# Kernel tuning notes

Hardware: AMD Instinct MI355X
Metric: run time of the kernel (lower is better)

The kernel has to match this reference:

```python
import jax, jax.numpy as jnp
import numpy as np

B, QL, KL = 2, 256, 256
QD, KD, H = 1024, 1024, 512
EPS = 1e-5


def setup_inputs() -> dict:
    key = jax.random.key(0)
    ks = jax.random.split(key, 12)
    s = lambda d: 1.0 / np.sqrt(d)
    return {
        "Q": jax.random.normal(ks[0], (B, QL, QD), jnp.float32),
        "K": jax.random.normal(ks[1], (B, KL, KD), jnp.float32),
        "Wq": jax.random.normal(ks[2], (H, QD), jnp.float32) * s(QD),
        "Wk": jax.random.normal(ks[3], (H, KD), jnp.float32) * s(KD),
        "ln_w": jnp.ones((3 * H,), jnp.float32),
        "ln_b": jnp.zeros((3 * H,), jnp.float32),
        "Wu": jax.random.normal(ks[4], (H, 3 * H), jnp.float32) * s(3 * H),
        "bu": jnp.zeros((H,), jnp.float32),
        "Wv": jax.random.normal(ks[5], (H, 3 * H), jnp.float32) * s(3 * H),
        "bv": jnp.zeros((H,), jnp.float32),
        "Wo": jax.random.normal(ks[6], (1, H), jnp.float32) * s(H),
        "bo": jnp.zeros((1,), jnp.float32),
    }


def reference(Q, K, Wq, Wk, ln_w, ln_b, Wu, bu, Wv, bv, Wo, bo):
    # project queries and keys to hidden
    q = jnp.einsum('bqd,hd->bqh', Q, Wq)          # (B,QL,H)
    k = jnp.einsum('bkd,hd->bkh', K, Wk)          # (B,KL,H)
    qe = jnp.broadcast_to(q[:, :, None, :], (B, QL, KL, H))
    ke = jnp.broadcast_to(k[:, None, :, :], (B, QL, KL, H))
    x = jnp.concatenate([qe, ke, qe * ke], axis=-1)   # (B,QL,KL,3H)
    # LayerNorm over last dim
    mu = jnp.mean(x, axis=-1, keepdims=True)
    var = jnp.mean((x - mu) ** 2, axis=-1, keepdims=True)
    x = (x - mu) * jax.lax.rsqrt(var + EPS) * ln_w + ln_b
    U = jnp.einsum('bqkc,hc->bqkh', x, Wu) + bu
    V = jnp.einsum('bqkc,hc->bqkh', x, Wv) + bv
    Z = U * jax.nn.gelu(V, approximate=False)
    s = jnp.einsum('bqkh,oh->bqko', Z, Wo) + bo
    return s[..., 0]                               # (B,QL,KL)
```

## Files before the change

### kernel.cpp

```cpp
#include <hip/hip_runtime.h>
#include <hip/hip_bf16.h>

#define QLEN 256
#define QD 1024
#define HD 512
#define H3 1536
#define EPSF 1e-5f

typedef __attribute__((ext_vector_type(8))) short short8;
typedef __attribute__((ext_vector_type(4))) float f32x4;

__device__ inline short f2bf(float f) {
    union { float f; unsigned u; } v; v.f = f;
    unsigned r = v.u + 0x7FFF + ((v.u >> 16) & 1);
    return (short)(r >> 16);
}
__device__ inline float bf2f(short s) {
    union { float f; unsigned u; } v; v.u = ((unsigned)(unsigned short)s) << 16;
    return v.f;
}
__device__ inline unsigned pk2(float a, float b) {
    return ((unsigned)(unsigned short)f2bf(a)) | (((unsigned)(unsigned short)f2bf(b)) << 16);
}
__device__ inline float asf(unsigned u) { union { unsigned u; float f; } v; v.u = u; return v.f; }
__device__ inline unsigned cvtpk(float lo, float hi) {
    unsigned r;
    asm("v_cvt_pk_bf16_f32 %0, %1, %2" : "=v"(r) : "v"(lo), "v"(hi));
    return r;
}

__global__ __launch_bounds__(256) void prep_w2(const float* __restrict__ Wu_, const float* __restrict__ Wv_,
                                               const float* __restrict__ lnw, const float* __restrict__ lnb,
                                               const float* __restrict__ bu_, const float* __restrict__ bv_,
                                               short* __restrict__ W1u, short* __restrict__ W2u, short* __restrict__ W3u,
                                               short* __restrict__ W1v, short* __restrict__ W2v, short* __restrict__ W3v,
                                               float* __restrict__ su, float* __restrict__ tu,
                                               float* __restrict__ sv, float* __restrict__ tv) {
    int h = blockIdx.x, z = blockIdx.y, tid = threadIdx.x;
    const float* row = (z ? Wv_ : Wu_) + (size_t)h * H3;
    const float* bias = z ? bv_ : bu_;
    short* W1 = z ? W1v : W1u; short* W2 = z ? W2v : W2u; short* W3 = z ? W3v : W3u;
    float* svec = z ? sv : su; float* tvec = z ? tv : tu;
    for (int j = tid; j < HD; j += 256) {
        W1[h * HD + j] = f2bf(lnw[j] * row[j]);
        W2[h * HD + j] = f2bf(lnw[HD + j] * row[HD + j]);
        W3[h * HD + j] = f2bf(lnw[2 * HD + j] * row[2 * HD + j]);
    }
    float s = 0.f, t = 0.f;
    for (int c = tid; c < H3; c += 256) {
        float w = row[c];
        s += lnw[c] * w;
        t += lnb[c] * w;
    }
    for (int m = 1; m < 64; m <<= 1) { s += __shfl_xor(s, m, 64); t += __shfl_xor(t, m, 64); }
    __shared__ float rs[4], rt[4];
    if ((tid & 63) == 0) { rs[tid >> 6] = s; rt[tid >> 6] = t; }
    __syncthreads();
    if (tid == 0) {
        svec[h] = rs[0] + rs[1] + rs[2] + rs[3];
        tvec[h] = rt[0] + rt[1] + rt[2] + rt[3] + bias[h];
    }
}

__global__ __launch_bounds__(256) void proj2(const float* __restrict__ Q_, const float* __restrict__ K_,
                                             const float* __restrict__ Wq_, const float* __restrict__ Wk_,
                                             short* __restrict__ qbf, short* __restrict__ kbf) {
    int z = blockIdx.z;
    const float* In = z ? K_ : Q_;
    const float* W = z ? Wk_ : Wq_;
    short* OutB = z ? kbf : qbf;
    __shared__ short a_l[64][72], b_l[64][72];
    int t = threadIdx.x;
    int i0 = blockIdx.y * 64, n0 = blockIdx.x * 64;
    int lane = t & 63, wv = t >> 6, wm = wv >> 1, wn = wv & 1;
    int l15 = lane & 15, lg = lane >> 4;
    f32x4 acc[2][2] = {};
    int sr = t >> 4, sc = (t & 15) * 4;
    for (int kc = 0; kc < QD; kc += 64) {
#pragma unroll
        for (int rep = 0; rep < 4; ++rep) {
            int row = sr + rep * 16;
            float4 av = *(const float4*)&In[(size_t)(i0 + row) * QD + kc + sc];
            float4 bv = *(const float4*)&W[(size_t)(n0 + row) * QD + kc + sc];
            *(uint2*)&a_l[row][sc] = (uint2){pk2(av.x, av.y), pk2(av.z, av.w)};
            *(uint2*)&b_l[row][sc] = (uint2){pk2(bv.x, bv.y), pk2(bv.z, bv.w)};
        }
        __syncthreads();
#pragma unroll
        for (int kk = 0; kk < 2; ++kk) {
            short8 af[2], bf_[2];
#pragma unroll
            for (int mi = 0; mi < 2; ++mi)
                af[mi] = *(const short8*)&a_l[wm * 32 + mi * 16 + l15][kk * 32 + lg * 8];
#pragma unroll
            for (int nj = 0; nj < 2; ++nj)
                bf_[nj] = *(const short8*)&b_l[wn * 32 + nj * 16 + l15][kk * 32 + lg * 8];
#pragma unroll
            for (int mi = 0; mi < 2; ++mi)
#pragma unroll
                for (int nj = 0; nj < 2; ++nj)
                    acc[mi][nj] = __builtin_amdgcn_mfma_f32_16x16x32_bf16(af[mi], bf_[nj], acc[mi][nj], 0, 0, 0);
        }
        __syncthreads();
    }
#pragma unroll
    for (int mi = 0; mi < 2; ++mi)
#pragma unroll
        for (int nj = 0; nj < 2; ++nj)
#pragma unroll
            for (int r = 0; r < 4; ++r) {
                int row = i0 + wm * 32 + mi * 16 + lg * 4 + r;
                int col = n0 + wn * 32 + nj * 16 + l15;
                OutB[(size_t)row * HD + col] = f2bf(acc[mi][nj][r]);
            }
}

__global__ __launch_bounds__(256) void rowstats2(const unsigned* __restrict__ qbf, const unsigned* __restrict__ kbf,
                                                 float* __restrict__ s1q, float* __restrict__ s2q,
                                                 float* __restrict__ s1k, float* __restrict__ s2k,
                                                 float* __restrict__ out, const float* __restrict__ bo) {
    int row = blockIdx.x, z = blockIdx.y, tid = threadIdx.x;
    int gid = (z * 512 + row) * 256 + tid;
    if (gid < 2 * QLEN * QLEN) out[gid] = bo[0];
    const unsigned* Xbf = z ? kbf : qbf;
    float* s1 = z ? s1k : s1q;
    float* s2 = z ? s2k : s2q;
    unsigned u = Xbf[row * 256 + tid];
    float a = bf2f((short)(u & 0xffff)), b = bf2f((short)(u >> 16));
    float s = a + b, q = a * a + b * b;
    for (int m = 1; m < 64; m <<= 1) { s += __shfl_xor(s, m, 64); q += __shfl_xor(q, m, 64); }
    __shared__ float rs[4], rq[4];
    if ((tid & 63) == 0) { rs[tid >> 6] = s; rq[tid >> 6] = q; }
    __syncthreads();
    if (tid == 0) {
        s1[row] = rs[0] + rs[1] + rs[2] + rs[3];
        s2[row] = rq[0] + rq[1] + rq[2] + rq[3];
    }
}

__global__ __launch_bounds__(256) void lnlin4(const short* __restrict__ qbf, const short* __restrict__ kbf,
                                              const short* __restrict__ W1u, const short* __restrict__ W1v,
                                              const short* __restrict__ W2u, const short* __restrict__ W2v,
                                              float* __restrict__ Au, float* __restrict__ Av,
                                              float* __restrict__ BuT, float* __restrict__ BvT) {
    int z = blockIdx.z;
    const short* A = (z < 2) ? qbf : kbf;
    const short* W = (z == 0) ? W1u : (z == 1) ? W1v : (z == 2) ? W2u : W2v;
    float* Out = (z == 0) ? Au : (z == 1) ? Av : (z == 2) ? BuT : BvT;
    bool tr = z >= 2;
    __shared__ short a_l[64][72], b_l[64][72];
    int t = threadIdx.x;
    int i0 = blockIdx.y * 64, n0 = blockIdx.x * 64;
    int lane = t & 63, wv = t >> 6, wm = wv >> 1, wn = wv & 1;
    int l15 = lane & 15, lg = lane >> 4;
    f32x4 acc[2][2] = {};
    int sr = t >> 4, sc = (t & 15) * 4;
    for (int kc = 0; kc < HD; kc += 64) {
#pragma unroll
        for (int rep = 0; rep < 4; ++rep) {
            int row = sr + rep * 16;
            *(uint2*)&a_l[row][sc] = *(const uint2*)&A[(size_t)(i0 + row) * HD + kc + sc];
            *(uint2*)&b_l[row][sc] = *(const uint2*)&W[(size_t)(n0 + row) * HD + kc + sc];
        }
        __syncthreads();
#pragma unroll
        for (int kk = 0; kk < 2; ++kk) {
            short8 af[2], bf_[2];
#pragma unroll
            for (int mi = 0; mi < 2; ++mi)
                af[mi] = *(const short8*)&a_l[wm * 32 + mi * 16 + l15][kk * 32 + lg * 8];
#pragma unroll
            for (int nj = 0; nj < 2; ++nj)
                bf_[nj] = *(const short8*)&b_l[wn * 32 + nj * 16 + l15][kk * 32 + lg * 8];
#pragma unroll
            for (int mi = 0; mi < 2; ++mi)
#pragma unroll
                for (int nj = 0; nj < 2; ++nj)
                    acc[mi][nj] = __builtin_amdgcn_mfma_f32_16x16x32_bf16(af[mi], bf_[nj], acc[mi][nj], 0, 0, 0);
        }
        __syncthreads();
    }
#pragma unroll
    for (int mi = 0; mi < 2; ++mi)
#pragma unroll
        for (int nj = 0; nj < 2; ++nj)
#pragma unroll
            for (int r = 0; r < 4; ++r) {
                int row = i0 + wm * 32 + mi * 16 + lg * 4 + r;
                int col = n0 + wn * 32 + nj * 16 + l15;
                if (tr) Out[(size_t)col * HD + row] = acc[mi][nj][r];
                else    Out[(size_t)row * HD + col] = acc[mi][nj][r];
            }
}

__global__ __launch_bounds__(512) void main2(const short* __restrict__ qbf,
                                             const short* __restrict__ kbf,
                                             const float* __restrict__ Au,
                                             const float* __restrict__ Av,
                                             const float* __restrict__ BuT,
                                             const float* __restrict__ BvT,
                                             const short* __restrict__ W3u,
                                             const short* __restrict__ W3v,
                                             const float* __restrict__ su,
                                             const float* __restrict__ tu,
                                             const float* __restrict__ sv,
                                             const float* __restrict__ tv,
                                             const float* __restrict__ Wo,
                                             const float* __restrict__ s1q,
                                             const float* __restrict__ s2q,
                                             const float* __restrict__ s1k,
                                             const float* __restrict__ s2k,
                                             float* __restrict__ out) {
    __shared__ short q_l[16 * 512];
    __shared__ short k_l[16 * 512];
    __shared__ short B_l[2][2][128 * 64];
    __shared__ float stat_l[512];
    __shared__ float sred[8][64];

    int tid = threadIdx.x;
    int kt = blockIdx.x, qt = blockIdx.y;
    int b = blockIdx.z >> 2, hs = blockIdx.z & 3;
    int qbase = qt * 16, kbase = kt * 16, hbase = hs * 128;
    int lane = tid & 63, wv = tid >> 6;
    int l15 = lane & 15, lg = lane >> 4;
    int wm = wv & 3, wn = wv >> 2;

    f32x4 accU[4][4], accV[4][4];
#pragma unroll
    for (int mf = 0; mf < 4; ++mf) {
        int qrow = b * QLEN + qbase + wm * 4 + mf;
#pragma unroll
        for (int nf = 0; nf < 4; ++nf) {
            int h = hbase + wn * 64 + nf * 16 + l15;
            float au = Au[(size_t)qrow * HD + h];
            float av = Av[(size_t)qrow * HD + h];
            f32x4 bu4 = *(const f32x4*)&BuT[(size_t)h * 512 + b * QLEN + kbase + lg * 4];
            f32x4 bv4 = *(const f32x4*)&BvT[(size_t)h * 512 + b * QLEN + kbase + lg * 4];
#pragma unroll
            for (int r = 0; r < 4; ++r) {
                accU[mf][nf][r] = au + bu4[r];
                accV[mf][nf][r] = av + bv4[r];
            }
        }
    }

    stat_l[tid] = 0.f;
    for (int i = tid; i < 2048; i += 512) {
        int tile = i >> 10, slot = i & 1023;
        int row = slot >> 6, col16 = slot & 63;
        const short* sp = (tile ? kbf : qbf) +
            (size_t)(b * QLEN + (tile ? kbase : qbase) + row) * HD + col16 * 8;
        uint4 v = *(const uint4*)sp;
        short* dl = tile ? k_l : q_l;
        unsigned off = row * 1024 + ((col16 * 16) ^ ((row & 7) << 4));
        *(uint4*)((char*)dl + off) = v;
    }

    uint4 rb[4];
    auto loadB = [&](int kc) {
#pragma unroll
        for (int s = 0; s < 4; ++s) {
            int idx = s * 512 + tid;
            int uvx = idx >> 10, in = idx & 1023;
            int r = in >> 3, c16 = in & 7;
            const short* src = (uvx ? W3v : W3u) + (size_t)(hbase + r) * HD + kc + c16 * 8;
            rb[s] = *(const uint4*)src;
        }
    };
    auto storeB = [&](int buf) {
#pragma unroll
        for (int s = 0; s < 4; ++s) {
            int idx = s * 512 + tid;
            int uvx = idx >> 10, in = idx & 1023;
            int r = in >> 3, c16 = in & 7;
            unsigned off = r * 128 + ((c16 * 16) ^ ((r & 7) << 4));
            *(uint4*)((char*)&B_l[buf][uvx][0] + off) = rb[s];
        }
    };

    loadB(0);

    for (int c = 0; c < 8; ++c) {
        storeB(c & 1);
        if (c < 7) loadB((c + 1) * 64);
        __syncthreads();

        if (c == 0) {
            f32x4 d1 = {0.f, 0.f, 0.f, 0.f}, d2 = {0.f, 0.f, 0.f, 0.f};
#pragma unroll
            for (int s = 0; s < 2; ++s) {
                int jb = (wv * 2 + s) * 64 + lg * 16;
                uint4 qfu = *(const uint4*)((const char*)q_l + l15 * 1024 + (jb ^ ((l15 & 7) << 4)));
                uint4 kfu = *(const uint4*)((const char*)k_l + l15 * 1024 + (jb ^ ((l15 & 7) << 4)));
                d1 = __builtin_amdgcn_mfma_f32_16x16x32_bf16(
                    *(short8*)&qfu, *(short8*)&kfu, d1, 0, 0, 0);
                uint4 q2u, k2u;
                unsigned* qp = (unsigned*)&qfu; unsigned* kp = (unsigned*)&kfu;
                unsigned* q2p = (unsigned*)&q2u; unsigned* k2p = (unsigned*)&k2u;
#pragma unroll
                for (int i = 0; i < 4; ++i) {
                    float ql = asf(qp[i] << 16), qh = asf(qp[i] & 0xFFFF0000u);
                    float kl = asf(kp[i] << 16), kh = asf(kp[i] & 0xFFFF0000u);
                    q2p[i] = cvtpk(ql * ql, qh * qh);
                    k2p[i] = cvtpk(kl * kl, kh * kh);
                }
                d2 = __builtin_amdgcn_mfma_f32_16x16x32_bf16(
                    *(short8*)&q2u, *(short8*)&k2u, d2, 0, 0, 0);
            }
#pragma unroll
            for (int r = 0; r < 4; ++r) {
                int p = (lg * 4 + r) * 16 + l15;
                atomicAdd(&stat_l[p], d1[r]);
                atomicAdd(&stat_l[256 + p], d2[r]);
            }
        }

        const char* blu = (const char*)&B_l[c & 1][0][0];
        const char* blv = (const char*)&B_l[c & 1][1][0];
#pragma unroll
        for (int ksub = 0; ksub < 2; ++ksub) {
            int jb = (c * 2 + ksub) * 64 + lg * 16;
            int bb = ksub * 64 + lg * 16;
            uint4 kfu = *(const uint4*)((const char*)k_l + l15 * 1024 + (jb ^ ((l15 & 7) << 4)));
            unsigned* kp = (unsigned*)&kfu;
            float klo[4], khi[4];
#pragma unroll
            for (int i = 0; i < 4; ++i) {
                klo[i] = asf(kp[i] << 16);
                khi[i] = asf(kp[i] & 0xFFFF0000u);
            }
            short8 af[4];
#pragma unroll
            for (int mf = 0; mf < 4; ++mf) {
                int qrow = wm * 4 + mf;
                uint4 qfu = *(const uint4*)((const char*)q_l + qrow * 1024 + (jb ^ ((qrow & 7) << 4)));
                unsigned* qp = (unsigned*)&qfu;
                uint4 afu;
                unsigned* ap = (unsigned*)&afu;
#pragma unroll
                for (int i = 0; i < 4; ++i) {
                    float ql = asf(qp[i] << 16), qh = asf(qp[i] & 0xFFFF0000u);
                    ap[i] = cvtpk(ql * klo[i], qh * khi[i]);
                }
                af[mf] = *(short8*)&afu;
            }
#pragma unroll
            for (int nf = 0; nf < 4; ++nf) {
                int row = wn * 64 + nf * 16 + l15;
                unsigned off = row * 128 + (bb ^ ((row & 7) << 4));
                short8 bu_f = *(const short8*)(blu + off);
                short8 bv_f = *(const short8*)(blv + off);
#pragma unroll
                for (int mf = 0; mf < 4; ++mf) {
                    accU[mf][nf] = __builtin_amdgcn_mfma_f32_16x16x32_bf16(af[mf], bu_f, accU[mf][nf], 0, 0, 0);
                    accV[mf][nf] = __builtin_amdgcn_mfma_f32_16x16x32_bf16(af[mf], bv_f, accV[mf][nf], 0, 0, 0);
                }
            }
        }
    }

    if (tid < 256) {
        int qi = tid >> 4, ki = tid & 15;
        float mu = (s1q[b * QLEN + qbase + qi] + s1k[b * QLEN + kbase + ki] + stat_l[tid]) * (1.f / H3);
        float ex2 = (s2q[b * QLEN + qbase + qi] + s2k[b * QLEN + kbase + ki] + stat_l[256 + tid]) * (1.f / H3);
        float ri = rsqrtf(ex2 - mu * mu + EPSF);
        stat_l[tid] = ri;
        stat_l[256 + tid] = ri * mu;
    }
    __syncthreads();

    float sacc[16];
#pragma unroll
    for (int i = 0; i < 16; ++i) sacc[i] = 0.f;
#pragma unroll
    for (int nf = 0; nf < 4; ++nf) {
        int h = hbase + wn * 64 + nf * 16 + l15;
        float suh = su[h], tuh = tu[h], svh = sv[h], tvh = tv[h], woh = Wo[h];
#pragma unroll
        for (int mf = 0; mf < 4; ++mf) {
            int pbase = (wm * 4 + mf) * 16 + lg * 4;
#pragma unroll
            for (int r = 0; r < 4; ++r) {
                float ri = stat_l[pbase + r];
                float rmu = stat_l[256 + pbase + r];
                float u = fmaf(ri, accU[mf][nf][r], tuh) - rmu * suh;
                float vx = fmaf(ri, accV[mf][nf][r], tvh) - rmu * svh;
                float x2 = vx * vx;
                float tt = vx * fmaf(0.0356774081f, x2, 0.7978845608f);
                float e2 = exp2f(tt * 2.885390082f);
                float ge = vx - vx / (e2 + 1.0f);
                sacc[mf * 4 + r] = fmaf(u * ge, woh, sacc[mf * 4 + r]);
            }
        }
    }

#pragma unroll
    for (int i = 0; i < 16; ++i) {
        float v = sacc[i];
        v += __shfl_xor(v, 1, 64);
        v += __shfl_xor(v, 2, 64);
        v += __shfl_xor(v, 4, 64);
        v += __shfl_xor(v, 8, 64);
        sacc[i] = v;
    }
    if (l15 == 0) {
#pragma unroll
        for (int mf = 0; mf < 4; ++mf)
#pragma unroll
            for (int r = 0; r < 4; ++r)
                sred[wv][mf * 16 + lg * 4 + r] = sacc[mf * 4 + r];
    }
    __syncthreads();
    if (tid < 256) {
        int wm_ = tid >> 6, within = tid & 63;
        float val = sred[wm_][within] + sred[wm_ + 4][within];
        int qi = wm_ * 4 + (within >> 4), ki = within & 15;
        atomicAdd(&out[(size_t)(b * QLEN + qbase + qi) * QLEN + kbase + ki], val);
    }
}

extern "C" void kernel_launch(void* const* d_in, const int* in_sizes, int n_in,
                              void* d_out, int out_size, void* d_ws, size_t ws_size,
                              hipStream_t stream) {
    const float* Q   = (const float*)d_in[0];
    const float* Kin = (const float*)d_in[1];
    const float* Wq  = (const float*)d_in[2];
    const float* Wk  = (const float*)d_in[3];
    const float* lnw = (const float*)d_in[4];
    const float* lnb = (const float*)d_in[5];
    const float* Wu  = (const float*)d_in[6];
    const float* bu  = (const float*)d_in[7];
    const float* Wv  = (const float*)d_in[8];
    const float* bv  = (const float*)d_in[9];
    const float* Wo  = (const float*)d_in[10];
    const float* bo  = (const float*)d_in[11];
    float* out = (float*)d_out;

    char* ws = (char*)d_ws;
    size_t off = 0;
    auto alloc = [&](size_t bytes) -> void* {
        void* p = ws + off;
        off += (bytes + 255) & ~(size_t)255;
        return p;
    };
    const size_t WB = (size_t)HD * HD * 2;
    short* W1u = (short*)alloc(WB); short* W2u = (short*)alloc(WB); short* W3u = (short*)alloc(WB);
    short* W1v = (short*)alloc(WB); short* W2v = (short*)alloc(WB); short* W3v = (short*)alloc(WB);
    short* qbf = (short*)alloc(WB); short* kbf = (short*)alloc(WB);
    float* su = (float*)alloc(HD * 4); float* tu = (float*)alloc(HD * 4);
    float* sv = (float*)alloc(HD * 4); float* tv = (float*)alloc(HD * 4);
    float* s1q = (float*)alloc(512 * 4); float* s2q = (float*)alloc(512 * 4);
    float* s1k = (float*)alloc(512 * 4); float* s2k = (float*)alloc(512 * 4);
    float* Au  = (float*)alloc((size_t)512 * HD * 4);
    float* Av  = (float*)alloc((size_t)512 * HD * 4);
    float* BuT = (float*)alloc((size_t)512 * HD * 4);
    float* BvT = (float*)alloc((size_t)512 * HD * 4);

    prep_w2<<<dim3(HD, 2), 256, 0, stream>>>(Wu, Wv, lnw, lnb, bu, bv,
                                             W1u, W2u, W3u, W1v, W2v, W3v, su, tu, sv, tv);

    proj2<<<dim3(8, 8, 2), 256, 0, stream>>>(Q, Kin, Wq, Wk, qbf, kbf);

    rowstats2<<<dim3(512, 2), 256, 0, stream>>>((const unsigned*)qbf, (const unsigned*)kbf,
                                                s1q, s2q, s1k, s2k, out, bo);

    lnlin4<<<dim3(8, 8, 4), 256, 0, stream>>>(qbf, kbf, W1u, W1v, W2u, W2v, Au, Av, BuT, BvT);

    main2<<<dim3(16, 16, 8), 512, 0, stream>>>(
        qbf, kbf, Au, Av, BuT, BvT, W3u, W3v, su, tu, sv, tv, Wo,
        s1q, s2q, s1k, s2k, out);
}
```

Measured before the change: 433.2 us.

## Switch to fp16 with packed products and pre-swizzled W3 fragments read directly

Changes every intermediate from bf16 to fp16. The q*k elementwise product is now a native packed half multiply instead of unpack, float multiply and repack. W3 is pre-permuted in prep into the MFMA fragment layout, so main2 reads B fragments straight from global memory, with no LDS staging, double buffering or syncs. The Au/Av/BuT/BvT loads move into the epilogue. fp16 has less range than bf16, and squared values or products could overflow, which is a risk for accuracy.

```diff
diff --git a/kernel.cpp b/kernel.cpp
--- a/kernel.cpp
+++ b/kernel.cpp
@@ -7,44 +7,34 @@
 #define H3 1536
 #define EPSF 1e-5f
 
-typedef __attribute__((ext_vector_type(8))) short short8;
+typedef __attribute__((ext_vector_type(8))) _Float16 half8;
 typedef __attribute__((ext_vector_type(4))) float f32x4;
 
-__device__ inline short f2bf(float f) {
-    union { float f; unsigned u; } v; v.f = f;
-    unsigned r = v.u + 0x7FFF + ((v.u >> 16) & 1);
-    return (short)(r >> 16);
-}
-__device__ inline float bf2f(short s) {
-    union { float f; unsigned u; } v; v.u = ((unsigned)(unsigned short)s) << 16;
-    return v.f;
-}
-__device__ inline unsigned pk2(float a, float b) {
-    return ((unsigned)(unsigned short)f2bf(a)) | (((unsigned)(unsigned short)f2bf(b)) << 16);
-}
-__device__ inline float asf(unsigned u) { union { unsigned u; float f; } v; v.u = u; return v.f; }
-__device__ inline unsigned cvtpk(float lo, float hi) {
-    unsigned r;
-    asm("v_cvt_pk_bf16_f32 %0, %1, %2" : "=v"(r) : "v"(lo), "v"(hi));
-    return r;
+__device__ inline short f2h(float f) { _Float16 h = (_Float16)f; return __builtin_bit_cast(short, h); }
+__device__ inline float h2f(short s) { return (float)__builtin_bit_cast(_Float16, s); }
+__device__ inline unsigned pkh(float a, float b) {
+    return __builtin_bit_cast(unsigned, __builtin_amdgcn_cvt_pkrtz(a, b));
 }
 
 __global__ __launch_bounds__(256) void prep_w2(const float* __restrict__ Wu_, const float* __restrict__ Wv_,
                                                const float* __restrict__ lnw, const float* __restrict__ lnb,
                                                const float* __restrict__ bu_, const float* __restrict__ bv_,
-                                               short* __restrict__ W1u, short* __restrict__ W2u, short* __restrict__ W3u,
-                                               short* __restrict__ W1v, short* __restrict__ W2v, short* __restrict__ W3v,
+                                               short* __restrict__ W1u, short* __restrict__ W2u, short* __restrict__ W3pu,
+                                               short* __restrict__ W1v, short* __restrict__ W2v, short* __restrict__ W3pv,
                                                float* __restrict__ su, float* __restrict__ tu,
                                                float* __restrict__ sv, float* __restrict__ tv) {
     int h = blockIdx.x, z = blockIdx.y, tid = threadIdx.x;
     const float* row = (z ? Wv_ : Wu_) + (size_t)h * H3;
     const float* bias = z ? bv_ : bu_;
-    short* W1 = z ? W1v : W1u; short* W2 = z ? W2v : W2u; short* W3 = z ? W3v : W3u;
+    short* W1 = z ? W1v : W1u; short* W2 = z ? W2v : W2u; short* W3p = z ? W3pv : W3pu;
     float* svec = z ? sv : su; float* tvec = z ? tv : tu;
+    int ht = h >> 4, l15h = h & 15;
     for (int j = tid; j < HD; j += 256) {
-        W1[h * HD + j] = f2bf(lnw[j] * row[j]);
-        W2[h * HD + j] = f2bf(lnw[HD + j] * row[HD + j]);
-        W3[h * HD + j] = f2bf(lnw[2 * HD + j] * row[2 * HD + j]);
+        W1[h * HD + j] = f2h(lnw[j] * row[j]);
+        W2[h * HD + j] = f2h(lnw[HD + j] * row[HD + j]);
+        float w3 = lnw[2 * HD + j] * row[2 * HD + j];
+        int ks = j >> 5, lg2 = (j >> 3) & 3, ii = j & 7;
+        W3p[((ht * 16 + ks) * 64 + lg2 * 16 + l15h) * 8 + ii] = f2h(w3);
     }
     float s = 0.f, t = 0.f;
     for (int c = tid; c < H3; c += 256) {
@@ -64,11 +54,11 @@
 
 __global__ __launch_bounds__(256) void proj2(const float* __restrict__ Q_, const float* __restrict__ K_,
                                              const float* __restrict__ Wq_, const float* __restrict__ Wk_,
-                                             short* __restrict__ qbf, short* __restrict__ kbf) {
+                                             short* __restrict__ qh, short* __restrict__ kh) {
     int z = blockIdx.z;
     const float* In = z ? K_ : Q_;
     const float* W = z ? Wk_ : Wq_;
-    short* OutB = z ? kbf : qbf;
+    short* OutB = z ? kh : qh;
     __shared__ short a_l[64][72], b_l[64][72];
     int t = threadIdx.x;
     int i0 = blockIdx.y * 64, n0 = blockIdx.x * 64;
@@ -82,24 +72,24 @@
             int row = sr + rep * 16;
             float4 av = *(const float4*)&In[(size_t)(i0 + row) * QD + kc + sc];
             float4 bv = *(const float4*)&W[(size_t)(n0 + row) * QD + kc + sc];
-            *(uint2*)&a_l[row][sc] = (uint2){pk2(av.x, av.y), pk2(av.z, av.w)};
-            *(uint2*)&b_l[row][sc] = (uint2){pk2(bv.x, bv.y), pk2(bv.z, bv.w)};
+            *(uint2*)&a_l[row][sc] = (uint2){pkh(av.x, av.y), pkh(av.z, av.w)};
+            *(uint2*)&b_l[row][sc] = (uint2){pkh(bv.x, bv.y), pkh(bv.z, bv.w)};
         }
         __syncthreads();
 #pragma unroll
         for (int kk = 0; kk < 2; ++kk) {
-            short8 af[2], bf_[2];
+            half8 af[2], bf_[2];
 #pragma unroll
             for (int mi = 0; mi < 2; ++mi)
-                af[mi] = *(const short8*)&a_l[wm * 32 + mi * 16 + l15][kk * 32 + lg * 8];
+                af[mi] = *(const half8*)&a_l[wm * 32 + mi * 16 + l15][kk * 32 + lg * 8];
 #pragma unroll
             for (int nj = 0; nj < 2; ++nj)
-                bf_[nj] = *(const short8*)&b_l[wn * 32 + nj * 16 + l15][kk * 32 + lg * 8];
+                bf_[nj] = *(const half8*)&b_l[wn * 32 + nj * 16 + l15][kk * 32 + lg * 8];
 #pragma unroll
             for (int mi = 0; mi < 2; ++mi)
 #pragma unroll
                 for (int nj = 0; nj < 2; ++nj)
-                    acc[mi][nj] = __builtin_amdgcn_mfma_f32_16x16x32_bf16(af[mi], bf_[nj], acc[mi][nj], 0, 0, 0);
+                    acc[mi][nj] = __builtin_amdgcn_mfma_f32_16x16x32_f16(af[mi], bf_[nj], acc[mi][nj], 0, 0, 0);
         }
         __syncthreads();
     }
@@ -111,22 +101,22 @@
             for (int r = 0; r < 4; ++r) {
                 int row = i0 + wm * 32 + mi * 16 + lg * 4 + r;
                 int col = n0 + wn * 32 + nj * 16 + l15;
-                OutB[(size_t)row * HD + col] = f2bf(acc[mi][nj][r]);
+                OutB[(size_t)row * HD + col] = f2h(acc[mi][nj][r]);
             }
 }
 
-__global__ __launch_bounds__(256) void rowstats2(const unsigned* __restrict__ qbf, const unsigned* __restrict__ kbf,
+__global__ __launch_bounds__(256) void rowstats2(const unsigned* __restrict__ qh, const unsigned* __restrict__ kh,
                                                  float* __restrict__ s1q, float* __restrict__ s2q,
                                                  float* __restrict__ s1k, float* __restrict__ s2k,
                                                  float* __restrict__ out, const float* __restrict__ bo) {
     int row = blockIdx.x, z = blockIdx.y, tid = threadIdx.x;
     int gid = (z * 512 + row) * 256 + tid;
     if (gid < 2 * QLEN * QLEN) out[gid] = bo[0];
-    const unsigned* Xbf = z ? kbf : qbf;
+    const unsigned* Xh = z ? kh : qh;
     float* s1 = z ? s1k : s1q;
     float* s2 = z ? s2k : s2q;
-    unsigned u = Xbf[row * 256 + tid];
-    float a = bf2f((short)(u & 0xffff)), b = bf2f((short)(u >> 16));
+    unsigned u = Xh[row * 256 + tid];
+    float a = h2f((short)(u & 0xffff)), b = h2f((short)(u >> 16));
     float s = a + b, q = a * a + b * b;
     for (int m = 1; m < 64; m <<= 1) { s += __shfl_xor(s, m, 64); q += __shfl_xor(q, m, 64); }
     __shared__ float rs[4], rq[4];
@@ -138,13 +128,13 @@
     }
 }
 
-__global__ __launch_bounds__(256) void lnlin4(const short* __restrict__ qbf, const short* __restrict__ kbf,
+__global__ __launch_bounds__(256) void lnlin4(const short* __restrict__ qh, const short* __restrict__ kh,
                                               const short* __restrict__ W1u, const short* __restrict__ W1v,
                                               const short* __restrict__ W2u, const short* __restrict__ W2v,
                                               float* __restrict__ Au, float* __restrict__ Av,
                                               float* __restrict__ BuT, float* __restrict__ BvT) {
     int z = blockIdx.z;
-    const short* A = (z < 2) ? qbf : kbf;
+    const short* A = (z < 2) ? qh : kh;
     const short* W = (z == 0) ? W1u : (z == 1) ? W1v : (z == 2) ? W2u : W2v;
     float* Out = (z == 0) ? Au : (z == 1) ? Av : (z == 2) ? BuT : BvT;
     bool tr = z >= 2;
@@ -165,18 +155,18 @@
         __syncthreads();
 #pragma unroll
         for (int kk = 0; kk < 2; ++kk) {
-            short8 af[2], bf_[2];
+            half8 af[2], bf_[2];
 #pragma unroll
             for (int mi = 0; mi < 2; ++mi)
-                af[mi] = *(const short8*)&a_l[wm * 32 + mi * 16 + l15][kk * 32 + lg * 8];
+                af[mi] = *(const half8*)&a_l[wm * 32 + mi * 16 + l15][kk * 32 + lg * 8];
 #pragma unroll
             for (int nj = 0; nj < 2; ++nj)
-                bf_[nj] = *(const short8*)&b_l[wn * 32 + nj * 16 + l15][kk * 32 + lg * 8];
+                bf_[nj] = *(const half8*)&b_l[wn * 32 + nj * 16 + l15][kk * 32 + lg * 8];
 #pragma unroll
             for (int mi = 0; mi < 2; ++mi)
 #pragma unroll
                 for (int nj = 0; nj < 2; ++nj)
-                    acc[mi][nj] = __builtin_amdgcn_mfma_f32_16x16x32_bf16(af[mi], bf_[nj], acc[mi][nj], 0, 0, 0);
+                    acc[mi][nj] = __builtin_amdgcn_mfma_f32_16x16x32_f16(af[mi], bf_[nj], acc[mi][nj], 0, 0, 0);
         }
         __syncthreads();
     }
@@ -193,14 +183,14 @@
             }
 }
 
-__global__ __launch_bounds__(512) void main2(const short* __restrict__ qbf,
-                                             const short* __restrict__ kbf,
+__global__ __launch_bounds__(512) void main2(const short* __restrict__ qh,
+                                             const short* __restrict__ kh,
                                              const float* __restrict__ Au,
                                              const float* __restrict__ Av,
                                              const float* __restrict__ BuT,
                                              const float* __restrict__ BvT,
-                                             const short* __restrict__ W3u,
-                                             const short* __restrict__ W3v,
+                                             const short* __restrict__ W3pu,
+                                             const short* __restrict__ W3pv,
                                              const float* __restrict__ su,
                                              const float* __restrict__ tu,
                                              const float* __restrict__ sv,
@@ -213,7 +203,6 @@
                                              float* __restrict__ out) {
     __shared__ short q_l[16 * 512];
     __shared__ short k_l[16 * 512];
-    __shared__ short B_l[2][2][128 * 64];
     __shared__ float stat_l[512];
     __shared__ float sred[8][64];
 
@@ -225,140 +214,68 @@
     int l15 = lane & 15, lg = lane >> 4;
     int wm = wv & 3, wn = wv >> 2;
 
-    f32x4 accU[4][4], accV[4][4];
-#pragma unroll
-    for (int mf = 0; mf < 4; ++mf) {
-        int qrow = b * QLEN + qbase + wm * 4 + mf;
-#pragma unroll
-        for (int nf = 0; nf < 4; ++nf) {
-            int h = hbase + wn * 64 + nf * 16 + l15;
-            float au = Au[(size_t)qrow * HD + h];
-            float av = Av[(size_t)qrow * HD + h];
-            f32x4 bu4 = *(const f32x4*)&BuT[(size_t)h * 512 + b * QLEN + kbase + lg * 4];
-            f32x4 bv4 = *(const f32x4*)&BvT[(size_t)h * 512 + b * QLEN + kbase + lg * 4];
-#pragma unroll
-            for (int r = 0; r < 4; ++r) {
-                accU[mf][nf][r] = au + bu4[r];
-                accV[mf][nf][r] = av + bv4[r];
-            }
-        }
-    }
-
     stat_l[tid] = 0.f;
     for (int i = tid; i < 2048; i += 512) {
         int tile = i >> 10, slot = i & 1023;
         int row = slot >> 6, col16 = slot & 63;
-        const short* sp = (tile ? kbf : qbf) +
+        const short* sp = (tile ? kh : qh) +
             (size_t)(b * QLEN + (tile ? kbase : qbase) + row) * HD + col16 * 8;
         uint4 v = *(const uint4*)sp;
         short* dl = tile ? k_l : q_l;
         unsigned off = row * 1024 + ((col16 * 16) ^ ((row & 7) << 4));
         *(uint4*)((char*)dl + off) = v;
     }
-
-    uint4 rb[4];
-    auto loadB = [&](int kc) {
-#pragma unroll
-        for (int s = 0; s < 4; ++s) {
-            int idx = s * 512 + tid;
-            int uvx = idx >> 10, in = idx & 1023;
-            int r = in >> 3, c16 = in & 7;
-            const short* src = (uvx ? W3v : W3u) + (size_t)(hbase + r) * HD + kc + c16 * 8;
-            rb[s] = *(const uint4*)src;
-        }
-    };
-    auto storeB = [&](int buf) {
-#pragma unroll
-        for (int s = 0; s < 4; ++s) {
-            int idx = s * 512 + tid;
-            int uvx = idx >> 10, in = idx & 1023;
-            int r = in >> 3, c16 = in & 7;
-            unsigned off = r * 128 + ((c16 * 16) ^ ((r & 7) << 4));
-            *(uint4*)((char*)&B_l[buf][uvx][0] + off) = rb[s];
-        }
-    };
-
-    loadB(0);
-
-    for (int c = 0; c < 8; ++c) {
-        storeB(c & 1);
-        if (c < 7) loadB((c + 1) * 64);
-        __syncthreads();
-
-        if (c == 0) {
-            f32x4 d1 = {0.f, 0.f, 0.f, 0.f}, d2 = {0.f, 0.f, 0.f, 0.f};
-#pragma unroll
-            for (int s = 0; s < 2; ++s) {
-                int jb = (wv * 2 + s) * 64 + lg * 16;
-                uint4 qfu = *(const uint4*)((const char*)q_l + l15 * 1024 + (jb ^ ((l15 & 7) << 4)));
-                uint4 kfu = *(const uint4*)((const char*)k_l + l15 * 1024 + (jb ^ ((l15 & 7) << 4)));
-                d1 = __builtin_amdgcn_mfma_f32_16x16x32_bf16(
-                    *(short8*)&qfu, *(short8*)&kfu, d1, 0, 0, 0);
-                uint4 q2u, k2u;
-                unsigned* qp = (unsigned*)&qfu; unsigned* kp = (unsigned*)&kfu;
-                unsigned* q2p = (unsigned*)&q2u; unsigned* k2p = (unsigned*)&k2u;
-#pragma unroll
-                for (int i = 0; i < 4; ++i) {
-                    float ql = asf(qp[i] << 16), qh = asf(qp[i] & 0xFFFF0000u);
-                    float kl = asf(kp[i] << 16), kh = asf(kp[i] & 0xFFFF0000u);
-                    q2p[i] = cvtpk(ql * ql, qh * qh);
-                    k2p[i] = cvtpk(kl * kl, kh * kh);
-                }
-                d2 = __builtin_amdgcn_mfma_f32_16x16x32_bf16(
-                    *(short8*)&q2u, *(short8*)&k2u, d2, 0, 0, 0);
+    __syncthreads();
+
+    {
+        f32x4 d1 = {0.f, 0.f, 0.f, 0.f}, d2 = {0.f, 0.f, 0.f, 0.f};
+#pragma unroll
+        for (int s = 0; s < 2; ++s) {
+            int jb = (wv * 2 + s) * 64 + lg * 16;
+            uint4 qfu = *(const uint4*)((const char*)q_l + l15 * 1024 + (jb ^ ((l15 & 7) << 4)));
+            uint4 kfu = *(const uint4*)((const char*)k_l + l15 * 1024 + (jb ^ ((l15 & 7) << 4)));
+            half8 q8 = __builtin_bit_cast(half8, qfu);
+            half8 k8 = __builtin_bit_cast(half8, kfu);
+            half8 q2 = q8 * q8, k2 = k8 * k8;
+            d1 = __builtin_amdgcn_mfma_f32_16x16x32_f16(q8, k8, d1, 0, 0, 0);
+            d2 = __builtin_amdgcn_mfma_f32_16x16x32_f16(q2, k2, d2, 0, 0, 0);
+        }
+#pragma unroll
+        for (int r = 0; r < 4; ++r) {
+            int p = (lg * 4 + r) * 16 + l15;
+            atomicAdd(&stat_l[p], d1[r]);
+            atomicAdd(&stat_l[256 + p], d2[r]);
+        }
+    }
+
+    f32x4 accU[4][4] = {}, accV[4][4] = {};
+    int ht0 = hs * 8 + wn * 4;
+#pragma unroll 2
+    for (int ks = 0; ks < 16; ++ks) {
+        int jb = ks * 64 + lg * 16;
+        uint4 kfu = *(const uint4*)((const char*)k_l + l15 * 1024 + (jb ^ ((l15 & 7) << 4)));
+        half8 k8 = __builtin_bit_cast(half8, kfu);
+        half8 af[4];
+#pragma unroll
+        for (int mf = 0; mf < 4; ++mf) {
+            int qrow = wm * 4 + mf;
+            uint4 qfu = *(const uint4*)((const char*)q_l + qrow * 1024 + (jb ^ ((qrow & 7) << 4)));
+            af[mf] = __builtin_bit_cast(half8, qfu) * k8;
+        }
+#pragma unroll
+        for (int nf = 0; nf < 4; ++nf) {
+            int fo = ((ht0 + nf) * 16 + ks) * 512 + lane * 8;
+            half8 bu = *(const half8*)(W3pu + fo);
+            half8 bv = *(const half8*)(W3pv + fo);
+#pragma unroll
+            for (int mf = 0; mf < 4; ++mf) {
+                accU[mf][nf] = __builtin_amdgcn_mfma_f32_16x16x32_f16(af[mf], bu, accU[mf][nf], 0, 0, 0);
+                accV[mf][nf] = __builtin_amdgcn_mfma_f32_16x16x32_f16(af[mf], bv, accV[mf][nf], 0, 0, 0);
             }
-#pragma unroll
-            for (int r = 0; r < 4; ++r) {
-                int p = (lg * 4 + r) * 16 + l15;
-                atomicAdd(&stat_l[p], d1[r]);
-                atomicAdd(&stat_l[256 + p], d2[r]);
-            }
-        }
-
-        const char* blu = (const char*)&B_l[c & 1][0][0];
-        const char* blv = (const char*)&B_l[c & 1][1][0];
-#pragma unroll
-        for (int ksub = 0; ksub < 2; ++ksub) {
-            int jb = (c * 2 + ksub) * 64 + lg * 16;
-            int bb = ksub * 64 + lg * 16;
-            uint4 kfu = *(const uint4*)((const char*)k_l + l15 * 1024 + (jb ^ ((l15 & 7) << 4)));
-            unsigned* kp = (unsigned*)&kfu;
-            float klo[4], khi[4];
-#pragma unroll
-            for (int i = 0; i < 4; ++i) {
-                klo[i] = asf(kp[i] << 16);
-                khi[i] = asf(kp[i] & 0xFFFF0000u);
-            }
-            short8 af[4];
-#pragma unroll
-            for (int mf = 0; mf < 4; ++mf) {
-                int qrow = wm * 4 + mf;
-                uint4 qfu = *(const uint4*)((const char*)q_l + qrow * 1024 + (jb ^ ((qrow & 7) << 4)));
-                unsigned* qp = (unsigned*)&qfu;
-                uint4 afu;
-                unsigned* ap = (unsigned*)&afu;
-#pragma unroll
-                for (int i = 0; i < 4; ++i) {
-                    float ql = asf(qp[i] << 16), qh = asf(qp[i] & 0xFFFF0000u);
-                    ap[i] = cvtpk(ql * klo[i], qh * khi[i]);
-                }
-                af[mf] = *(short8*)&afu;
-            }
-#pragma unroll
-            for (int nf = 0; nf < 4; ++nf) {
-                int row = wn * 64 + nf * 16 + l15;
-                unsigned off = row * 128 + (bb ^ ((row & 7) << 4));
-                short8 bu_f = *(const short8*)(blu + off);
-                short8 bv_f = *(const short8*)(blv + off);
-#pragma unroll
-                for (int mf = 0; mf < 4; ++mf) {
-                    accU[mf][nf] = __builtin_amdgcn_mfma_f32_16x16x32_bf16(af[mf], bu_f, accU[mf][nf], 0, 0, 0);
-                    accV[mf][nf] = __builtin_amdgcn_mfma_f32_16x16x32_bf16(af[mf], bv_f, accV[mf][nf], 0, 0, 0);
-                }
-            }
-        }
-    }
-
+        }
+    }
+
+    __syncthreads();
     if (tid < 256) {
         int qi = tid >> 4, ki = tid & 15;
         float mu = (s1q[b * QLEN + qbase + qi] + s1k[b * QLEN + kbase + ki] + stat_l[tid]) * (1.f / H3);
@@ -376,15 +293,22 @@
     for (int nf = 0; nf < 4; ++nf) {
         int h = hbase + wn * 64 + nf * 16 + l15;
         float suh = su[h], tuh = tu[h], svh = sv[h], tvh = tv[h], woh = Wo[h];
+        f32x4 bu4 = *(const f32x4*)&BuT[(size_t)h * 512 + b * QLEN + kbase + lg * 4];
+        f32x4 bv4 = *(const f32x4*)&BvT[(size_t)h * 512 + b * QLEN + kbase + lg * 4];
 #pragma unroll
         for (int mf = 0; mf < 4; ++mf) {
+            int qrow = b * QLEN + qbase + wm * 4 + mf;
+            float au = Au[(size_t)qrow * HD + h];
+            float av = Av[(size_t)qrow * HD + h];
             int pbase = (wm * 4 + mf) * 16 + lg * 4;
 #pragma unroll
             for (int r = 0; r < 4; ++r) {
                 float ri = stat_l[pbase + r];
                 float rmu = stat_l[256 + pbase + r];
-                float u = fmaf(ri, accU[mf][nf][r], tuh) - rmu * suh;
-                float vx = fmaf(ri, accV[mf][nf][r], tvh) - rmu * svh;
+                float gu = au + bu4[r] + accU[mf][nf][r];
+                float gv = av + bv4[r] + accV[mf][nf][r];
+                float u = fmaf(ri, gu, tuh) - rmu * suh;
+                float vx = fmaf(ri, gv, tvh) - rmu * svh;
                 float x2 = vx * vx;
                 float tt = vx * fmaf(0.0356774081f, x2, 0.7978845608f);
                 float e2 = exp2f(tt * 2.885390082f);
@@ -444,9 +368,9 @@
         return p;
     };
     const size_t WB = (size_t)HD * HD * 2;
-    short* W1u = (short*)alloc(WB); short* W2u = (short*)alloc(WB); short* W3u = (short*)alloc(WB);
-    short* W1v = (short*)alloc(WB); short* W2v = (short*)alloc(WB); short* W3v = (short*)alloc(WB);
-    short* qbf = (short*)alloc(WB); short* kbf = (short*)alloc(WB);
+    short* W1u = (short*)alloc(WB); short* W2u = (short*)alloc(WB); short* W3pu = (short*)alloc(WB);
+    short* W1v = (short*)alloc(WB); short* W2v = (short*)alloc(WB); short* W3pv = (short*)alloc(WB);
+    short* qh = (short*)alloc(WB); short* kh = (short*)alloc(WB);
     float* su = (float*)alloc(HD * 4); float* tu = (float*)alloc(HD * 4);
     float* sv = (float*)alloc(HD * 4); float* tv = (float*)alloc(HD * 4);
     float* s1q = (float*)alloc(512 * 4); float* s2q = (float*)alloc(512 * 4);
@@ -457,16 +381,16 @@
     float* BvT = (float*)alloc((size_t)512 * HD * 4);
 
     prep_w2<<<dim3(HD, 2), 256, 0, stream>>>(Wu, Wv, lnw, lnb, bu, bv,
-                                             W1u, W2u, W3u, W1v, W2v, W3v, su, tu, sv, tv);
-
-    proj2<<<dim3(8, 8, 2), 256, 0, stream>>>(Q, Kin, Wq, Wk, qbf, kbf);
-
-    rowstats2<<<dim3(512, 2), 256, 0, stream>>>((const unsigned*)qbf, (const unsigned*)kbf,
+                                             W1u, W2u, W3pu, W1v, W2v, W3pv, su, tu, sv, tv);
+
+    proj2<<<dim3(8, 8, 2), 256, 0, stream>>>(Q, Kin, Wq, Wk, qh, kh);
+
+    rowstats2<<<dim3(512, 2), 256, 0, stream>>>((const unsigned*)qh, (const unsigned*)kh,
                                                 s1q, s2q, s1k, s2k, out, bo);
 
-    lnlin4<<<dim3(8, 8, 4), 256, 0, stream>>>(qbf, kbf, W1u, W1v, W2u, W2v, Au, Av, BuT, BvT);
+    lnlin4<<<dim3(8, 8, 4), 256, 0, stream>>>(qh, kh, W1u, W1v, W2u, W2v, Au, Av, BuT, BvT);
 
     main2<<<dim3(16, 16, 8), 512, 0, stream>>>(
-        qbf, kbf, Au, Av, BuT, BvT, W3u, W3v, su, tu, sv, tv, Wo,
+        qh, kh, Au, Av, BuT, BvT, W3pu, W3pv, su, tu, sv, tv, Wo,
         s1q, s2q, s1k, s2k, out);
 }
```

Result: faster. 380.0 us (-12.3%).
